# Optimization experiments

Measured on AMD Instinct MI355X. Metric: run time of the kernel, lower is better.

The kernel has to match this reference:

```python
import jax, jax.numpy as jnp
import numpy as np

B, S, H, HD = 2, 4096, 8, 64
D = H * HD
EPS = 1e-5

def setup_inputs() -> dict:
    key = jax.random.key(0)
    ks = jax.random.split(key, 8)
    sc = 0.05
    return {
        "x": jax.random.normal(ks[0], (B, S, D), jnp.float32),
        "y": jax.random.normal(ks[1], (B, S, D), jnp.float32),
        "Wk": jax.random.normal(ks[2], (H, HD, HD), jnp.float32) * sc,
        "bk": jax.random.normal(ks[3], (H, HD), jnp.float32) * sc,
        "Wq": jax.random.normal(ks[4], (H, HD, HD), jnp.float32) * sc,
        "bq": jax.random.normal(ks[5], (H, HD), jnp.float32) * sc,
        "Wv": jax.random.normal(ks[6], (H, HD, HD), jnp.float32) * sc,
        "bv": jax.random.normal(ks[7], (H, HD), jnp.float32) * sc,
        "gamma": jnp.ones((D,), jnp.float32),
        "beta": jnp.zeros((D,), jnp.float32),
    }

def reference(x, y, Wk, bk, Wq, bq, Wv, bv, gamma, beta):
    b, s, d = x.shape
    # slice-per-head == reshape to [B,S,H,HD]
    xh = x.reshape(b, s, H, HD)
    yh = y.reshape(b, s, H, HD)
    # per-head linear projections (batched over heads)
    K = jnp.einsum('bshd,hde->bshe', xh, Wk) + bk  # [B,S,H,HD]
    Q = jnp.einsum('bshd,hde->bshe', yh, Wq) + bq
    V = jnp.einsum('bshd,hde->bshe', xh, Wv) + bv
    scale = 1.0 / jnp.sqrt(jnp.float32(HD))
    scores = jnp.einsum('bshe,bthe->bhst', Q, K) * scale  # [B,H,S,S]
    attn = jax.nn.softmax(scores, axis=-1)
    out = jnp.einsum('bhst,bthe->bshe', attn, V)  # [B,S,H,HD]
    out = out.reshape(b, s, d) + y
    # LayerNorm over last dim
    mu = jnp.mean(out, axis=-1, keepdims=True)
    var = jnp.mean(jnp.square(out - mu), axis=-1, keepdims=True)
    return (out - mu) * jax.lax.rsqrt(var + EPS) * gamma + beta
```

## Files before the change

kernel.cpp:

```cpp
#include <hip/hip_runtime.h>
#include <hip/hip_bf16.h>

#define B_  2
#define S_  4096
#define H_  8
#define HD_ 64
#define D_  512
#define NSPLIT 2
#define NT_ ((S_ / NSPLIT) / 64)

using bf16x8 = __attribute__((ext_vector_type(8))) short;
using f32x4  = __attribute__((ext_vector_type(4))) float;
using f32x16 = __attribute__((ext_vector_type(16))) float;
using u32x4  = __attribute__((ext_vector_type(4))) unsigned int;

__device__ __forceinline__ unsigned short f2bf(float f) {
    unsigned int u = __float_as_uint(f);
    u += 0x7FFFu + ((u >> 16) & 1u);
    return (unsigned short)(u >> 16);
}

__device__ __forceinline__ float bf2f(short s) {
    return __uint_as_float(((unsigned int)(unsigned short)s) << 16);
}

__device__ __forceinline__ unsigned int pkbf(float a, float b) {
    unsigned int r;
    asm("v_cvt_pk_bf16_f32 %0, %1, %2" : "=v"(r) : "v"(a), "v"(b));
    return r;
}

__device__ __forceinline__ float ex2(float x) {
    float r;
    asm("v_exp_f32 %0, %1" : "=v"(r) : "v"(x));
    return r;
}

__device__ __forceinline__ void gl16(const unsigned short* g, unsigned short* l) {
    __builtin_amdgcn_global_load_lds(
        (const __attribute__((address_space(1))) unsigned int*)g,
        (__attribute__((address_space(3))) unsigned int*)l, 16, 0, 0);
}

__global__ __launch_bounds__(256) void proj_kernel(
    const float* __restrict__ x,  const float* __restrict__ yy,
    const float* __restrict__ Wk, const float* __restrict__ bk,
    const float* __restrict__ Wq, const float* __restrict__ bq,
    const float* __restrict__ Wv, const float* __restrict__ bv,
    unsigned short* __restrict__ Qw, unsigned short* __restrict__ Kw,
    unsigned short* __restrict__ Vt)
{
    __shared__ __attribute__((aligned(16))) unsigned short xs[64][72];
    __shared__ __attribute__((aligned(16))) unsigned short ys[64][72];
    __shared__ __attribute__((aligned(16))) unsigned short wtk[64][72];
    __shared__ __attribute__((aligned(16))) unsigned short wtq[64][72];
    __shared__ __attribute__((aligned(16))) unsigned short wtv[64][72];
    __shared__ __attribute__((aligned(16))) unsigned short vtl[64][72];

    const int t  = threadIdx.x;
    const int s0 = blockIdx.x * 64;
    const int bh = blockIdx.y;
    const int b  = bh >> 3, h = bh & 7;

    #pragma unroll
    for (int i = 0; i < 4; ++i) {
        int id = t + 256 * i;
        int row = id >> 4, c4 = id & 15;
        size_t ga = ((size_t)(b * S_ + s0 + row)) * D_ + h * HD_ + c4 * 4;
        float4 xv = *(const float4*)(x + ga);
        float4 yv = *(const float4*)(yy + ga);
        unsigned int xl = f2bf(xv.x) | ((unsigned int)f2bf(xv.y) << 16);
        unsigned int xh = f2bf(xv.z) | ((unsigned int)f2bf(xv.w) << 16);
        unsigned int yl = f2bf(yv.x) | ((unsigned int)f2bf(yv.y) << 16);
        unsigned int yh = f2bf(yv.z) | ((unsigned int)f2bf(yv.w) << 16);
        *(uint2*)&xs[row][c4 * 4] = make_uint2(xl, xh);
        *(uint2*)&ys[row][c4 * 4] = make_uint2(yl, yh);
    }
    #pragma unroll
    for (int i = 0; i < 4; ++i) {
        int id = t + 256 * i;
        int dd = id >> 4, e4 = id & 15;
        size_t wa = (size_t)(h * HD_ + dd) * HD_ + e4 * 4;
        float4 wk4 = *(const float4*)(Wk + wa);
        float4 wq4 = *(const float4*)(Wq + wa);
        float4 wv4 = *(const float4*)(Wv + wa);
        wtk[e4*4+0][dd] = f2bf(wk4.x); wtk[e4*4+1][dd] = f2bf(wk4.y);
        wtk[e4*4+2][dd] = f2bf(wk4.z); wtk[e4*4+3][dd] = f2bf(wk4.w);
        wtq[e4*4+0][dd] = f2bf(wq4.x); wtq[e4*4+1][dd] = f2bf(wq4.y);
        wtq[e4*4+2][dd] = f2bf(wq4.z); wtq[e4*4+3][dd] = f2bf(wq4.w);
        wtv[e4*4+0][dd] = f2bf(wv4.x); wtv[e4*4+1][dd] = f2bf(wv4.y);
        wtv[e4*4+2][dd] = f2bf(wv4.z); wtv[e4*4+3][dd] = f2bf(wv4.w);
    }
    __syncthreads();

    const int lane = t & 63, w = t >> 6;
    const int g = lane >> 4, lq = lane & 15;

    bf16x8 ax[2], ay[2];
    #pragma unroll
    for (int kk = 0; kk < 2; ++kk) {
        ax[kk] = *(const bf16x8*)&xs[w*16 + lq][kk*32 + g*8];
        ay[kk] = *(const bf16x8*)&ys[w*16 + lq][kk*32 + g*8];
    }
    __syncthreads();

    f32x4 ak[4], aq[4], av[4];
    #pragma unroll
    for (int n = 0; n < 4; ++n) { ak[n] = (f32x4)0.f; aq[n] = (f32x4)0.f; av[n] = (f32x4)0.f; }

    #pragma unroll
    for (int n = 0; n < 4; ++n) {
        #pragma unroll
        for (int kk = 0; kk < 2; ++kk) {
            bf16x8 bk_ = *(const bf16x8*)&wtk[n*16 + lq][kk*32 + g*8];
            ak[n] = __builtin_amdgcn_mfma_f32_16x16x32_bf16(ax[kk], bk_, ak[n], 0, 0, 0);
            bf16x8 bq_ = *(const bf16x8*)&wtq[n*16 + lq][kk*32 + g*8];
            aq[n] = __builtin_amdgcn_mfma_f32_16x16x32_bf16(ay[kk], bq_, aq[n], 0, 0, 0);
            bf16x8 bv_ = *(const bf16x8*)&wtv[n*16 + lq][kk*32 + g*8];
            av[n] = __builtin_amdgcn_mfma_f32_16x16x32_bf16(ax[kk], bv_, av[n], 0, 0, 0);
        }
    }

    const float cscale = 0.125f * 1.44269504088896340736f;
    #pragma unroll
    for (int n = 0; n < 4; ++n) {
        int e = n*16 + lq;
        float bkv = bk[h*HD_ + e], bqv = bq[h*HD_ + e], bvv = bv[h*HD_ + e];
        #pragma unroll
        for (int r = 0; r < 4; ++r) {
            int srow = w*16 + g*4 + r;
            xs[srow][e]  = f2bf(ak[n][r] + bkv);
            ys[srow][e]  = f2bf((aq[n][r] + bqv) * cscale);
            vtl[e][srow] = f2bf(av[n][r] + bvv);
        }
    }
    __syncthreads();
    #pragma unroll
    for (int i = 0; i < 2; ++i) {
        int id = t + 256 * i;
        int rr = id >> 3, c = id & 7;
        bf16x8 kv = *(const bf16x8*)&xs[rr][c*8];
        *(bf16x8*)(Kw + ((size_t)bh * S_ + s0 + rr) * HD_ + c*8) = kv;
        bf16x8 qv = *(const bf16x8*)&ys[rr][c*8];
        *(bf16x8*)(Qw + ((size_t)bh * S_ + s0 + rr) * HD_ + c*8) = qv;
        bf16x8 vv = *(const bf16x8*)&vtl[rr][c*8];
        *(bf16x8*)(Vt + ((size_t)bh * HD_ + rr) * S_ + s0 + c*8) = vv;
    }
}

__global__ __launch_bounds__(256, 4) void attn_kernel(
    const unsigned short* __restrict__ Qw, const unsigned short* __restrict__ Kw,
    const unsigned short* __restrict__ Vt, unsigned short* __restrict__ U,
    float* __restrict__ sbuf)
{
    __shared__ __attribute__((aligned(16))) unsigned short ksh[2][64][64];
    __shared__ __attribute__((aligned(16))) unsigned short vsh[2][64][64];

    const int t = threadIdx.x, lane = t & 63, w = t >> 6;
    const int lx = lane & 31, hi = lane >> 5;
    const int q0 = blockIdx.x * 128;
    const int bh = blockIdx.y;
    const int z  = blockIdx.z;
    const int b  = bh >> 3, h = bh & 7;
    const int kvbase = z * (S_ / NSPLIT);

    const unsigned short* Kb = Kw + ((size_t)bh * S_ + kvbase) * HD_;
    const unsigned short* Vb = Vt + (size_t)bh * HD_ * S_ + kvbase;

    bf16x8 qf[4];
    #pragma unroll
    for (int kq = 0; kq < 4; ++kq)
        qf[kq] = *(const bf16x8*)(Qw + ((size_t)bh*S_ + q0 + w*32 + lx)*HD_ + kq*16 + hi*8);

    f32x16 oaccT[2];
    oaccT[0] = (f32x16)0.f; oaccT[1] = (f32x16)0.f;
    float ssA = 0.f, ssB = 0.f;

    const int w16 = w * 16;
    const int sw8 = ((lane & 7) ^ (lane >> 3)) * 8;
    const unsigned short* kg0 = Kb + (size_t)(w16 +     (lane >> 3)) * HD_ + sw8;
    const unsigned short* kg1 = Kb + (size_t)(w16 + 8 + (lane >> 3)) * HD_ + sw8;
    const unsigned short* vg0 = Vb + (size_t)(w16 +     (lane >> 3)) * S_  + sw8;
    const unsigned short* vg1 = Vb + (size_t)(w16 + 8 + (lane >> 3)) * S_  + sw8;

    gl16(kg0, &ksh[0][w16][0]);     gl16(kg1, &ksh[0][w16 + 8][0]);
    gl16(vg0, &vsh[0][w16][0]);     gl16(vg1, &vsh[0][w16 + 8][0]);
    kg0 += 64 * HD_; kg1 += 64 * HD_; vg0 += 64; vg1 += 64;
    __syncthreads();

#define TILE(CUR, KT)                                                         \
    {                                                                         \
        if ((KT) + 1 < NT_) {                                                 \
            gl16(kg0, &ksh[(CUR)^1][w16][0]);                                 \
            gl16(kg1, &ksh[(CUR)^1][w16 + 8][0]);                             \
            gl16(vg0, &vsh[(CUR)^1][w16][0]);                                 \
            gl16(vg1, &vsh[(CUR)^1][w16 + 8][0]);                             \
            kg0 += 64 * HD_; kg1 += 64 * HD_; vg0 += 64; vg1 += 64;           \
        }                                                                     \
        __builtin_amdgcn_s_setprio(1);                                        \
        f32x16 st0 = (f32x16)0.f, st1 = (f32x16)0.f;                          \
        _Pragma("unroll")                                                     \
        for (int kq = 0; kq < 4; ++kq) {                                      \
            bf16x8 kf0 = *(const bf16x8*)&ksh[CUR][lx][(kq*16 + hi*8) ^ ((lx & 7)*8)]; \
            st0 = __builtin_amdgcn_mfma_f32_32x32x16_bf16(kf0, qf[kq], st0, 0, 0, 0);  \
            bf16x8 kf1 = *(const bf16x8*)&ksh[CUR][32 + lx][(kq*16 + hi*8) ^ ((lx & 7)*8)]; \
            st1 = __builtin_amdgcn_mfma_f32_32x32x16_bf16(kf1, qf[kq], st1, 0, 0, 0);  \
        }                                                                     \
        float ta = 0.f, tb = 0.f;                                             \
        _Pragma("unroll")                                                     \
        for (int r = 0; r < 16; ++r) {                                        \
            st0[r] = ex2(st0[r]); st1[r] = ex2(st1[r]);                       \
            ta += st0[r]; tb += st1[r];                                       \
        }                                                                     \
        ssA += ta; ssB += tb;                                                 \
        _Pragma("unroll")                                                     \
        for (int ks = 0; ks < 4; ++ks) {                                      \
            const int u0 = (ks & 1) * 2;                                      \
            unsigned int w0, w1, w2, w3;                                      \
            if (ks < 2) {                                                     \
                w0 = pkbf(st0[4*u0+0],     st0[4*u0+1]);                      \
                w2 = pkbf(st0[4*(u0+1)+0], st0[4*(u0+1)+1]);                  \
                w1 = pkbf(st0[4*u0+2],     st0[4*u0+3]);                      \
                w3 = pkbf(st0[4*(u0+1)+2], st0[4*(u0+1)+3]);                  \
            } else {                                                          \
                w0 = pkbf(st1[4*u0+0],     st1[4*u0+1]);                      \
                w2 = pkbf(st1[4*(u0+1)+0], st1[4*(u0+1)+1]);                  \
                w1 = pkbf(st1[4*u0+2],     st1[4*u0+3]);                      \
                w3 = pkbf(st1[4*(u0+1)+2], st1[4*(u0+1)+3]);                  \
            }                                                                 \
            asm("v_permlane32_swap_b32 %0, %1" : "+v"(w0), "+v"(w2));         \
            asm("v_permlane32_swap_b32 %0, %1" : "+v"(w1), "+v"(w3));         \
            u32x4 pw; pw.x = w0; pw.y = w1; pw.z = w2; pw.w = w3;             \
            bf16x8 pB = __builtin_bit_cast(bf16x8, pw);                       \
            _Pragma("unroll")                                                 \
            for (int d0 = 0; d0 < 2; ++d0) {                                  \
                const int vrow = d0*32 + lx;                                  \
                bf16x8 vf = *(const bf16x8*)&vsh[CUR][vrow][(ks*16 + hi*8) ^ ((vrow & 7)*8)]; \
                oaccT[d0] = __builtin_amdgcn_mfma_f32_32x32x16_bf16(vf, pB, oaccT[d0], 0, 0, 0); \
            }                                                                 \
        }                                                                     \
        __builtin_amdgcn_s_setprio(0);                                        \
        __syncthreads();                                                      \
    }

    for (int kt = 0; kt < NT_; kt += 2) {
        TILE(0, kt)
        TILE(1, kt + 1)
    }
#undef TILE

    float ssum = ssA + ssB;
    ssum += __shfl_xor(ssum, 32);
    unsigned short* osh = &ksh[0][0][0] + w * (32 * 64);
    #pragma unroll
    for (int d0 = 0; d0 < 2; ++d0)
        #pragma unroll
        for (int u = 0; u < 4; ++u) {
            unsigned int lo = pkbf(oaccT[d0][4*u+0], oaccT[d0][4*u+1]);
            unsigned int hw = pkbf(oaccT[d0][4*u+2], oaccT[d0][4*u+3]);
            int d = d0*32 + 8*u + 4*hi;
            *(uint2*)&osh[lx*64 + (d ^ ((lx & 7)*8))] = make_uint2(lo, hw);
        }
    __syncthreads();
    {
        const int rloc = lane >> 3;
        const int dcol = (lane & 7) * 8;
        unsigned short* ubase = U + (size_t)z * (B_*S_*(size_t)D_)
                                  + ((size_t)b * S_ + q0 + w*32) * D_ + h * HD_;
        #pragma unroll
        for (int i = 0; i < 4; ++i) {
            int q = i*8 + rloc;
            bf16x8 ov = *(const bf16x8*)&osh[q*64 + (dcol ^ ((q & 7)*8))];
            *(bf16x8*)(ubase + (size_t)q * D_ + dcol) = ov;
        }
    }
    if (hi == 0) {
        const int qrow = q0 + w*32 + lx;
        sbuf[(size_t)z * (B_*S_*H_) + ((size_t)b * S_ + qrow) * H_ + h] = ssum;
    }
}

__global__ __launch_bounds__(256) void ln_kernel(
    const unsigned short* __restrict__ U, const float* __restrict__ sbuf,
    const float* __restrict__ yy,
    const float* __restrict__ gamma, const float* __restrict__ beta,
    float* __restrict__ out)
{
    const int t = threadIdx.x, lane = t & 63, w = t >> 6;
    const size_t row = (size_t)blockIdx.x * 4 + w;
    const int h = lane >> 3;

    float s0 = sbuf[row * H_ + h];
    float s1 = sbuf[(size_t)(B_*S_)*H_ + row * H_ + h];
    float inv = 1.0f / (s0 + s1);

    bf16x8 u0 = *(const bf16x8*)(U + row * D_ + lane*8);
    bf16x8 u1 = *(const bf16x8*)(U + (size_t)(B_*S_)*(size_t)D_ + row * D_ + lane*8);
    const float* yr = yy + row * D_;

    float v[8];
    #pragma unroll
    for (int i = 0; i < 2; ++i) {
        float4 yv = *(const float4*)(yr + lane*8 + i*4);
        v[i*4+0] = (bf2f(u0[i*4+0]) + bf2f(u1[i*4+0]))*inv + yv.x;
        v[i*4+1] = (bf2f(u0[i*4+1]) + bf2f(u1[i*4+1]))*inv + yv.y;
        v[i*4+2] = (bf2f(u0[i*4+2]) + bf2f(u1[i*4+2]))*inv + yv.z;
        v[i*4+3] = (bf2f(u0[i*4+3]) + bf2f(u1[i*4+3]))*inv + yv.w;
    }
    float s = 0.f;
    #pragma unroll
    for (int j = 0; j < 8; ++j) s += v[j];
    #pragma unroll
    for (int o = 32; o >= 1; o >>= 1) s += __shfl_xor(s, o);
    float mu = s * (1.f / 512.f);
    float qs = 0.f;
    #pragma unroll
    for (int j = 0; j < 8; ++j) { float d = v[j] - mu; qs += d * d; }
    #pragma unroll
    for (int o = 32; o >= 1; o >>= 1) qs += __shfl_xor(qs, o);
    float rstd = rsqrtf(qs * (1.f / 512.f) + 1e-5f);

    #pragma unroll
    for (int i = 0; i < 2; ++i) {
        float4 gm = *(const float4*)(gamma + lane*8 + i*4);
        float4 bt = *(const float4*)(beta  + lane*8 + i*4);
        float4 o4;
        o4.x = (v[i*4+0] - mu) * rstd * gm.x + bt.x;
        o4.y = (v[i*4+1] - mu) * rstd * gm.y + bt.y;
        o4.z = (v[i*4+2] - mu) * rstd * gm.z + bt.z;
        o4.w = (v[i*4+3] - mu) * rstd * gm.w + bt.w;
        *(float4*)(out + row * D_ + lane*8 + i*4) = o4;
    }
}

extern "C" void kernel_launch(void* const* d_in, const int* in_sizes, int n_in,
                              void* d_out, int out_size, void* d_ws, size_t ws_size,
                              hipStream_t stream) {
    const float* x     = (const float*)d_in[0];
    const float* y     = (const float*)d_in[1];
    const float* Wk    = (const float*)d_in[2];
    const float* bk    = (const float*)d_in[3];
    const float* Wq    = (const float*)d_in[4];
    const float* bq    = (const float*)d_in[5];
    const float* Wv    = (const float*)d_in[6];
    const float* bv    = (const float*)d_in[7];
    const float* gamma = (const float*)d_in[8];
    const float* beta  = (const float*)d_in[9];

    const size_t NTOK = (size_t)B_ * H_ * S_ * HD_;
    unsigned short* Qw = (unsigned short*)d_ws;
    unsigned short* Kw = Qw + NTOK;
    unsigned short* Vt = Kw + NTOK;
    unsigned short* U  = Vt + NTOK;
    float* sbuf = (float*)(U + (size_t)NSPLIT * B_ * S_ * D_);

    dim3 pgrid(S_ / 64, B_ * H_);
    proj_kernel<<<pgrid, 256, 0, stream>>>(x, y, Wk, bk, Wq, bq, Wv, bv, Qw, Kw, Vt);
    dim3 agrid(S_ / 128, B_ * H_, NSPLIT);
    attn_kernel<<<agrid, 256, 0, stream>>>(Qw, Kw, Vt, U, sbuf);
    ln_kernel<<<(B_ * S_) / 4, 256, 0, stream>>>(U, sbuf, y, gamma, beta, (float*)d_out);
}
```

Measured before the change: 105.8 us.

## Process 64 query rows per wave to reuse K/V fragments across two MFMA groups

Doubles the query tile per block to 256 rows, with each wave computing two 32-row query groups against the same K and V fragments loaded from shared memory. This halves LDS reads per MFMA and halves the number of K/V tile loads across the grid. In exchange it uses more accumulator registers, lowers the occupancy bound to 2 blocks, and halves the number of blocks. The epilogue writes the two groups sequentially through per-wave shared scratch.

```diff
diff --git a/kernel.cpp b/kernel.cpp
--- a/kernel.cpp
+++ b/kernel.cpp
@@ -148,17 +148,16 @@
     }
 }
 
-__global__ __launch_bounds__(256, 4) void attn_kernel(
+__global__ __launch_bounds__(256, 2) void attn_kernel(
     const unsigned short* __restrict__ Qw, const unsigned short* __restrict__ Kw,
     const unsigned short* __restrict__ Vt, unsigned short* __restrict__ U,
     float* __restrict__ sbuf)
 {
-    __shared__ __attribute__((aligned(16))) unsigned short ksh[2][64][64];
-    __shared__ __attribute__((aligned(16))) unsigned short vsh[2][64][64];
+    __shared__ __attribute__((aligned(16))) unsigned short smem[4][64][64];
 
     const int t = threadIdx.x, lane = t & 63, w = t >> 6;
     const int lx = lane & 31, hi = lane >> 5;
-    const int q0 = blockIdx.x * 128;
+    const int q0 = blockIdx.x * 256;
     const int bh = blockIdx.y;
     const int z  = blockIdx.z;
     const int b  = bh >> 3, h = bh & 7;
@@ -167,13 +166,15 @@
     const unsigned short* Kb = Kw + ((size_t)bh * S_ + kvbase) * HD_;
     const unsigned short* Vb = Vt + (size_t)bh * HD_ * S_ + kvbase;
 
-    bf16x8 qf[4];
-    #pragma unroll
-    for (int kq = 0; kq < 4; ++kq)
-        qf[kq] = *(const bf16x8*)(Qw + ((size_t)bh*S_ + q0 + w*32 + lx)*HD_ + kq*16 + hi*8);
-
-    f32x16 oaccT[2];
-    oaccT[0] = (f32x16)0.f; oaccT[1] = (f32x16)0.f;
+    bf16x8 qfA[4], qfB[4];
+    #pragma unroll
+    for (int kq = 0; kq < 4; ++kq) {
+        qfA[kq] = *(const bf16x8*)(Qw + ((size_t)bh*S_ + q0 + w*64 + lx)*HD_ + kq*16 + hi*8);
+        qfB[kq] = *(const bf16x8*)(Qw + ((size_t)bh*S_ + q0 + w*64 + 32 + lx)*HD_ + kq*16 + hi*8);
+    }
+
+    f32x16 oA0 = (f32x16)0.f, oA1 = (f32x16)0.f;
+    f32x16 oB0 = (f32x16)0.f, oB1 = (f32x16)0.f;
     float ssA = 0.f, ssB = 0.f;
 
     const int w16 = w * 16;
@@ -183,61 +184,77 @@
     const unsigned short* vg0 = Vb + (size_t)(w16 +     (lane >> 3)) * S_  + sw8;
     const unsigned short* vg1 = Vb + (size_t)(w16 + 8 + (lane >> 3)) * S_  + sw8;
 
-    gl16(kg0, &ksh[0][w16][0]);     gl16(kg1, &ksh[0][w16 + 8][0]);
-    gl16(vg0, &vsh[0][w16][0]);     gl16(vg1, &vsh[0][w16 + 8][0]);
+    gl16(kg0, &smem[0][w16][0]);     gl16(kg1, &smem[0][w16 + 8][0]);
+    gl16(vg0, &smem[2][w16][0]);     gl16(vg1, &smem[2][w16 + 8][0]);
     kg0 += 64 * HD_; kg1 += 64 * HD_; vg0 += 64; vg1 += 64;
     __syncthreads();
 
 #define TILE(CUR, KT)                                                         \
     {                                                                         \
         if ((KT) + 1 < NT_) {                                                 \
-            gl16(kg0, &ksh[(CUR)^1][w16][0]);                                 \
-            gl16(kg1, &ksh[(CUR)^1][w16 + 8][0]);                             \
-            gl16(vg0, &vsh[(CUR)^1][w16][0]);                                 \
-            gl16(vg1, &vsh[(CUR)^1][w16 + 8][0]);                             \
+            gl16(kg0, &smem[(CUR)^1][w16][0]);                                \
+            gl16(kg1, &smem[(CUR)^1][w16 + 8][0]);                            \
+            gl16(vg0, &smem[2+((CUR)^1)][w16][0]);                            \
+            gl16(vg1, &smem[2+((CUR)^1)][w16 + 8][0]);                        \
             kg0 += 64 * HD_; kg1 += 64 * HD_; vg0 += 64; vg1 += 64;           \
         }                                                                     \
         __builtin_amdgcn_s_setprio(1);                                        \
-        f32x16 st0 = (f32x16)0.f, st1 = (f32x16)0.f;                          \
+        f32x16 sA0 = (f32x16)0.f, sA1 = (f32x16)0.f;                          \
+        f32x16 sB0 = (f32x16)0.f, sB1 = (f32x16)0.f;                          \
         _Pragma("unroll")                                                     \
         for (int kq = 0; kq < 4; ++kq) {                                      \
-            bf16x8 kf0 = *(const bf16x8*)&ksh[CUR][lx][(kq*16 + hi*8) ^ ((lx & 7)*8)]; \
-            st0 = __builtin_amdgcn_mfma_f32_32x32x16_bf16(kf0, qf[kq], st0, 0, 0, 0);  \
-            bf16x8 kf1 = *(const bf16x8*)&ksh[CUR][32 + lx][(kq*16 + hi*8) ^ ((lx & 7)*8)]; \
-            st1 = __builtin_amdgcn_mfma_f32_32x32x16_bf16(kf1, qf[kq], st1, 0, 0, 0);  \
-        }                                                                     \
-        float ta = 0.f, tb = 0.f;                                             \
+            bf16x8 kf0 = *(const bf16x8*)&smem[CUR][lx][(kq*16 + hi*8) ^ ((lx & 7)*8)]; \
+            sA0 = __builtin_amdgcn_mfma_f32_32x32x16_bf16(kf0, qfA[kq], sA0, 0, 0, 0); \
+            sB0 = __builtin_amdgcn_mfma_f32_32x32x16_bf16(kf0, qfB[kq], sB0, 0, 0, 0); \
+            bf16x8 kf1 = *(const bf16x8*)&smem[CUR][32 + lx][(kq*16 + hi*8) ^ ((lx & 7)*8)]; \
+            sA1 = __builtin_amdgcn_mfma_f32_32x32x16_bf16(kf1, qfA[kq], sA1, 0, 0, 0); \
+            sB1 = __builtin_amdgcn_mfma_f32_32x32x16_bf16(kf1, qfB[kq], sB1, 0, 0, 0); \
+        }                                                                     \
+        float tA = 0.f, tB = 0.f;                                             \
         _Pragma("unroll")                                                     \
         for (int r = 0; r < 16; ++r) {                                        \
-            st0[r] = ex2(st0[r]); st1[r] = ex2(st1[r]);                       \
-            ta += st0[r]; tb += st1[r];                                       \
-        }                                                                     \
-        ssA += ta; ssB += tb;                                                 \
+            sA0[r] = ex2(sA0[r]); sA1[r] = ex2(sA1[r]);                       \
+            sB0[r] = ex2(sB0[r]); sB1[r] = ex2(sB1[r]);                       \
+            tA += sA0[r] + sA1[r]; tB += sB0[r] + sB1[r];                     \
+        }                                                                     \
+        ssA += tA; ssB += tB;                                                 \
         _Pragma("unroll")                                                     \
         for (int ks = 0; ks < 4; ++ks) {                                      \
             const int u0 = (ks & 1) * 2;                                      \
-            unsigned int w0, w1, w2, w3;                                      \
+            unsigned int a0, a1, a2, a3, b0, b1, b2, b3;                      \
             if (ks < 2) {                                                     \
-                w0 = pkbf(st0[4*u0+0],     st0[4*u0+1]);                      \
-                w2 = pkbf(st0[4*(u0+1)+0], st0[4*(u0+1)+1]);                  \
-                w1 = pkbf(st0[4*u0+2],     st0[4*u0+3]);                      \
-                w3 = pkbf(st0[4*(u0+1)+2], st0[4*(u0+1)+3]);                  \
+                a0 = pkbf(sA0[4*u0+0],     sA0[4*u0+1]);                      \
+                a2 = pkbf(sA0[4*(u0+1)+0], sA0[4*(u0+1)+1]);                  \
+                a1 = pkbf(sA0[4*u0+2],     sA0[4*u0+3]);                      \
+                a3 = pkbf(sA0[4*(u0+1)+2], sA0[4*(u0+1)+3]);                  \
+                b0 = pkbf(sB0[4*u0+0],     sB0[4*u0+1]);                      \
+                b2 = pkbf(sB0[4*(u0+1)+0], sB0[4*(u0+1)+1]);                  \
+                b1 = pkbf(sB0[4*u0+2],     sB0[4*u0+3]);                      \
+                b3 = pkbf(sB0[4*(u0+1)+2], sB0[4*(u0+1)+3]);                  \
             } else {                                                          \
-                w0 = pkbf(st1[4*u0+0],     st1[4*u0+1]);                      \
-                w2 = pkbf(st1[4*(u0+1)+0], st1[4*(u0+1)+1]);                  \
-                w1 = pkbf(st1[4*u0+2],     st1[4*u0+3]);                      \
-                w3 = pkbf(st1[4*(u0+1)+2], st1[4*(u0+1)+3]);                  \
+                a0 = pkbf(sA1[4*u0+0],     sA1[4*u0+1]);                      \
+                a2 = pkbf(sA1[4*(u0+1)+0], sA1[4*(u0+1)+1]);                  \
+                a1 = pkbf(sA1[4*u0+2],     sA1[4*u0+3]);                      \
+                a3 = pkbf(sA1[4*(u0+1)+2], sA1[4*(u0+1)+3]);                  \
+                b0 = pkbf(sB1[4*u0+0],     sB1[4*u0+1]);                      \
+                b2 = pkbf(sB1[4*(u0+1)+0], sB1[4*(u0+1)+1]);                  \
+                b1 = pkbf(sB1[4*u0+2],     sB1[4*u0+3]);                      \
+                b3 = pkbf(sB1[4*(u0+1)+2], sB1[4*(u0+1)+3]);                  \
             }                                                                 \
-            asm("v_permlane32_swap_b32 %0, %1" : "+v"(w0), "+v"(w2));         \
-            asm("v_permlane32_swap_b32 %0, %1" : "+v"(w1), "+v"(w3));         \
-            u32x4 pw; pw.x = w0; pw.y = w1; pw.z = w2; pw.w = w3;             \
-            bf16x8 pB = __builtin_bit_cast(bf16x8, pw);                       \
-            _Pragma("unroll")                                                 \
-            for (int d0 = 0; d0 < 2; ++d0) {                                  \
-                const int vrow = d0*32 + lx;                                  \
-                bf16x8 vf = *(const bf16x8*)&vsh[CUR][vrow][(ks*16 + hi*8) ^ ((vrow & 7)*8)]; \
-                oaccT[d0] = __builtin_amdgcn_mfma_f32_32x32x16_bf16(vf, pB, oaccT[d0], 0, 0, 0); \
-            }                                                                 \
+            asm("v_permlane32_swap_b32 %0, %1" : "+v"(a0), "+v"(a2));         \
+            asm("v_permlane32_swap_b32 %0, %1" : "+v"(a1), "+v"(a3));         \
+            asm("v_permlane32_swap_b32 %0, %1" : "+v"(b0), "+v"(b2));         \
+            asm("v_permlane32_swap_b32 %0, %1" : "+v"(b1), "+v"(b3));         \
+            u32x4 pwA; pwA.x = a0; pwA.y = a1; pwA.z = a2; pwA.w = a3;        \
+            u32x4 pwB; pwB.x = b0; pwB.y = b1; pwB.z = b2; pwB.w = b3;        \
+            bf16x8 pA = __builtin_bit_cast(bf16x8, pwA);                      \
+            bf16x8 pB = __builtin_bit_cast(bf16x8, pwB);                      \
+            bf16x8 vf0 = *(const bf16x8*)&smem[2+(CUR)][lx][(ks*16 + hi*8) ^ ((lx & 7)*8)]; \
+            bf16x8 vf1 = *(const bf16x8*)&smem[2+(CUR)][32 + lx][(ks*16 + hi*8) ^ (((32+lx) & 7)*8)]; \
+            oA0 = __builtin_amdgcn_mfma_f32_32x32x16_bf16(vf0, pA, oA0, 0, 0, 0); \
+            oB0 = __builtin_amdgcn_mfma_f32_32x32x16_bf16(vf0, pB, oB0, 0, 0, 0); \
+            oA1 = __builtin_amdgcn_mfma_f32_32x32x16_bf16(vf1, pA, oA1, 0, 0, 0); \
+            oB1 = __builtin_amdgcn_mfma_f32_32x32x16_bf16(vf1, pB, oB1, 0, 0, 0); \
         }                                                                     \
         __builtin_amdgcn_s_setprio(0);                                        \
         __syncthreads();                                                      \
@@ -249,35 +266,40 @@
     }
 #undef TILE
 
-    float ssum = ssA + ssB;
-    ssum += __shfl_xor(ssum, 32);
-    unsigned short* osh = &ksh[0][0][0] + w * (32 * 64);
-    #pragma unroll
-    for (int d0 = 0; d0 < 2; ++d0)
-        #pragma unroll
-        for (int u = 0; u < 4; ++u) {
-            unsigned int lo = pkbf(oaccT[d0][4*u+0], oaccT[d0][4*u+1]);
-            unsigned int hw = pkbf(oaccT[d0][4*u+2], oaccT[d0][4*u+3]);
-            int d = d0*32 + 8*u + 4*hi;
-            *(uint2*)&osh[lx*64 + (d ^ ((lx & 7)*8))] = make_uint2(lo, hw);
-        }
-    __syncthreads();
-    {
-        const int rloc = lane >> 3;
-        const int dcol = (lane & 7) * 8;
-        unsigned short* ubase = U + (size_t)z * (B_*S_*(size_t)D_)
-                                  + ((size_t)b * S_ + q0 + w*32) * D_ + h * HD_;
-        #pragma unroll
-        for (int i = 0; i < 4; ++i) {
-            int q = i*8 + rloc;
-            bf16x8 ov = *(const bf16x8*)&osh[q*64 + (dcol ^ ((q & 7)*8))];
-            *(bf16x8*)(ubase + (size_t)q * D_ + dcol) = ov;
-        }
-    }
-    if (hi == 0) {
-        const int qrow = q0 + w*32 + lx;
-        sbuf[(size_t)z * (B_*S_*H_) + ((size_t)b * S_ + qrow) * H_ + h] = ssum;
-    }
+    ssA += __shfl_xor(ssA, 32);
+    ssB += __shfl_xor(ssB, 32);
+    unsigned short* osh = &smem[0][0][0] + w * 4096;
+    const int rloc = lane >> 3;
+    const int dcol = (lane & 7) * 8;
+
+#define OUT_GROUP(OG0, OG1, SS, G32)                                          \
+    {                                                                         \
+        _Pragma("unroll")                                                     \
+        for (int d0 = 0; d0 < 2; ++d0)                                        \
+            _Pragma("unroll")                                                 \
+            for (int u = 0; u < 4; ++u) {                                     \
+                unsigned int lo = pkbf((d0 ? OG1 : OG0)[4*u+0], (d0 ? OG1 : OG0)[4*u+1]); \
+                unsigned int hw = pkbf((d0 ? OG1 : OG0)[4*u+2], (d0 ? OG1 : OG0)[4*u+3]); \
+                int d = d0*32 + 8*u + 4*hi;                                   \
+                *(uint2*)&osh[lx*64 + (d ^ ((lx & 7)*8))] = make_uint2(lo, hw); \
+            }                                                                 \
+        unsigned short* ubase = U + (size_t)z * (B_*S_*(size_t)D_)            \
+                                  + ((size_t)b * S_ + q0 + w*64 + (G32)) * D_ + h * HD_; \
+        _Pragma("unroll")                                                     \
+        for (int i = 0; i < 4; ++i) {                                         \
+            int q = i*8 + rloc;                                               \
+            bf16x8 ov = *(const bf16x8*)&osh[q*64 + (dcol ^ ((q & 7)*8))];    \
+            *(bf16x8*)(ubase + (size_t)q * D_ + dcol) = ov;                   \
+        }                                                                     \
+        if (hi == 0) {                                                        \
+            const int qrow = q0 + w*64 + (G32) + lx;                          \
+            sbuf[(size_t)z * (B_*S_*H_) + ((size_t)b * S_ + qrow) * H_ + h] = (SS); \
+        }                                                                     \
+    }
+
+    OUT_GROUP(oA0, oA1, ssA, 0)
+    OUT_GROUP(oB0, oB1, ssB, 32)
+#undef OUT_GROUP
 }
 
 __global__ __launch_bounds__(256) void ln_kernel(
@@ -356,7 +378,7 @@
 
     dim3 pgrid(S_ / 64, B_ * H_);
     proj_kernel<<<pgrid, 256, 0, stream>>>(x, y, Wk, bk, Wq, bq, Wv, bv, Qw, Kw, Vt);
-    dim3 agrid(S_ / 128, B_ * H_, NSPLIT);
+    dim3 agrid(S_ / 256, B_ * H_, NSPLIT);
     attn_kernel<<<agrid, 256, 0, stream>>>(Qw, Kw, Vt, U, sbuf);
     ln_kernel<<<(B_ * S_) / 4, 256, 0, stream>>>(U, sbuf, y, gamma, beta, (float*)d_out);
 }
```

Measured after the change: 96.91 us (median of 2 runs). 8.4% less time.
